# Kernel optimization log

Hardware: AMD Instinct MI355X
Metric: run time of the kernel (lower is better)

The kernel has to match this reference:

```python
import jax, jax.numpy as jnp
import numpy as np

B, C, H, W = 8, 128, 64, 64


def setup_inputs() -> dict:
    key = jax.random.key(0)
    ks = jax.random.split(key, 4)
    s = 1.0 / np.sqrt(C)
    return {
        "x": jax.random.normal(ks[0], (B, C, H, W), dtype=jnp.float32),
        "Wq": jax.random.normal(ks[1], (C, C), dtype=jnp.float32) * s,
        "bq": jnp.zeros((C,), dtype=jnp.float32),
        "Wk": jax.random.normal(ks[2], (C, C), dtype=jnp.float32) * s,
        "bk": jnp.zeros((C,), dtype=jnp.float32),
        "Wv": jax.random.normal(ks[3], (C, C), dtype=jnp.float32) * s,
        "bv": jnp.zeros((C,), dtype=jnp.float32),
    }


def reference(x, Wq, bq, Wk, bk, Wv, bv):
    b, c, h, w = x.shape
    xf = x.reshape(b, c, h * w)  # [B, C, N]
    # 1x1 convs are per-pixel CxC matmuls (weight[out,in] contracted over in)
    q = jnp.einsum("oc,bcn->bon", Wq, xf) + bq[None, :, None]
    k = jnp.einsum("oc,bcn->bon", Wk, xf) + bk[None, :, None]
    v = jnp.einsum("oc,bcn->bon", Wv, xf) + bv[None, :, None]
    scale = 1.0 / jnp.sqrt(jnp.asarray(c, dtype=x.dtype))
    attn = jnp.einsum("bcn,bcm->bnm", q, k) * scale  # [B, N, N]
    attn = jax.nn.softmax(attn, axis=-1)
    out = jnp.einsum("bnm,bcm->bcn", attn, v)  # [B, C, N]
    return out.reshape(b, c, h, w) + x
```

## Files before the change

### kernel.cpp

```cpp
#include <hip/hip_runtime.h>

#define B_ 8
#define C_ 128
#define N_ 4096
#define SCALE 0.08838834764831845f

typedef __attribute__((ext_vector_type(8))) short short8;
typedef __attribute__((ext_vector_type(4))) short short4v;
typedef __attribute__((ext_vector_type(4))) float f32x4;

__device__ inline float b2f(unsigned short u) {
    union { unsigned int i; float f; } v; v.i = ((unsigned int)u) << 16; return v.f;
}
__device__ inline unsigned short f2b(float f) {
    unsigned int x = __float_as_uint(f);
    return (unsigned short)((x + 0x7FFFu + ((x >> 16) & 1u)) >> 16);
}

__device__ inline void gld_lds16(const void* g, void* l) {
    __builtin_amdgcn_global_load_lds(
        (const __attribute__((address_space(1))) unsigned int*)g,
        (__attribute__((address_space(3))) unsigned int*)l, 16, 0, 0);
}

__global__ __launch_bounds__(256) void qkv_mfma(
    const float* __restrict__ x,
    const float* __restrict__ Wq, const float* __restrict__ bq,
    const float* __restrict__ Wk, const float* __restrict__ bk,
    const float* __restrict__ Wv, const float* __restrict__ bv,
    float* __restrict__ q, unsigned short* __restrict__ kTs,
    unsigned short* __restrict__ vS)
{
    __shared__ __align__(16) short Xs[64 * 128];
    __shared__ __align__(16) float Obuf[64 * 132];

    const int t    = threadIdx.x;
    const int w    = t >> 6;
    const int lane = t & 63;
    const int l15  = lane & 15;
    const int quad = lane >> 4;

    const int b  = blockIdx.x & 7;
    const int n0 = (blockIdx.x >> 3) * 64;
    const long base = (long)b * C_ * N_;

    auto load_af = [&](const float* __restrict__ W, short8 (&af)[2][4]) {
        #pragma unroll
        for (int ot = 0; ot < 2; ++ot) {
            const int o = 32 * w + 16 * ot + l15;
            #pragma unroll
            for (int ks = 0; ks < 4; ++ks) {
                const float4 a0 = *(const float4*)(const void*)(W + o * C_ + ks * 32 + quad * 8);
                const float4 a1 = *(const float4*)(const void*)(W + o * C_ + ks * 32 + quad * 8 + 4);
                short8 f;
                f[0] = (short)f2b(a0.x); f[1] = (short)f2b(a0.y);
                f[2] = (short)f2b(a0.z); f[3] = (short)f2b(a0.w);
                f[4] = (short)f2b(a1.x); f[5] = (short)f2b(a1.y);
                f[6] = (short)f2b(a1.z); f[7] = (short)f2b(a1.w);
                af[ot][ks] = f;
            }
        }
    };

    auto mfma_pass = [&](const short8 (&af)[2][4], f32x4 (&acc)[2][4]) {
        #pragma unroll
        for (int ot = 0; ot < 2; ++ot)
            #pragma unroll
            for (int nt = 0; nt < 4; ++nt)
                acc[ot][nt] = (f32x4){0.f, 0.f, 0.f, 0.f};
        #pragma unroll
        for (int nt = 0; nt < 4; ++nt) {
            const int n = nt * 16 + l15;
            short8 bx[4];
            #pragma unroll
            for (int ks = 0; ks < 4; ++ks)
                bx[ks] = *(const short8*)(const void*)(Xs + n * 128 + (((ks * 4 + quad) ^ l15) << 3));
            #pragma unroll
            for (int ot = 0; ot < 2; ++ot)
                #pragma unroll
                for (int ks = 0; ks < 4; ++ks)
                    acc[ot][nt] = __builtin_amdgcn_mfma_f32_16x16x32_bf16(af[ot][ks], bx[ks], acc[ot][nt], 0, 0, 0);
        }
    };

    short8 afA[2][4], afB[2][4];
    load_af(Wq, afA);

    #pragma unroll
    for (int it = 0; it < 8; ++it) {
        const int c  = (t >> 4) + it * 16;
        const int n4 = (t & 15) * 4;
        const float4 xv = *(const float4*)(const void*)(x + base + (long)c * N_ + n0 + n4);
        const int bc = c >> 3, cl = c & 7;
        Xs[(n4 + 0) * 128 + ((bc ^ ((n4 + 0) & 15)) << 3) + cl] = (short)f2b(xv.x);
        Xs[(n4 + 1) * 128 + ((bc ^ ((n4 + 1) & 15)) << 3) + cl] = (short)f2b(xv.y);
        Xs[(n4 + 2) * 128 + ((bc ^ ((n4 + 2) & 15)) << 3) + cl] = (short)f2b(xv.z);
        Xs[(n4 + 3) * 128 + ((bc ^ ((n4 + 3) & 15)) << 3) + cl] = (short)f2b(xv.w);
    }
    __syncthreads();

    {
        load_af(Wv, afB);
        f32x4 acc[2][4];
        mfma_pass(afA, acc);
        #pragma unroll
        for (int ot = 0; ot < 2; ++ot)
            #pragma unroll
            for (int r = 0; r < 4; ++r) {
                const int o = 32 * w + 16 * ot + quad * 4 + r;
                const float bb = bq[o];
                #pragma unroll
                for (int nt = 0; nt < 4; ++nt)
                    q[base + (long)o * N_ + n0 + nt * 16 + l15] = (acc[ot][nt][r] + bb) * SCALE;
            }
    }

    {
        load_af(Wk, afA);
        f32x4 acc[2][4];
        mfma_pass(afB, acc);
        #pragma unroll
        for (int ot = 0; ot < 2; ++ot)
            #pragma unroll
            for (int r = 0; r < 4; ++r) {
                const int o = 32 * w + 16 * ot + quad * 4 + r;
                const float bb = bv[o];
                const int sw = ((o >> 1) & 3) << 3;
                #pragma unroll
                for (int nt = 0; nt < 4; ++nt) {
                    const int n = nt * 16 + l15;
                    const int ns = (n & 32) | ((((n >> 3) & 3) << 3) ^ sw) | (n & 7);
                    vS[base + (long)o * N_ + n0 + ns] = f2b(acc[ot][nt][r] + bb);
                }
            }
    }

    {
        f32x4 acc[2][4];
        mfma_pass(afA, acc);
        #pragma unroll
        for (int ot = 0; ot < 2; ++ot)
            #pragma unroll
            for (int r = 0; r < 4; ++r) {
                const int o = 32 * w + 16 * ot + quad * 4 + r;
                const float bb = bk[o];
                #pragma unroll
                for (int nt = 0; nt < 4; ++nt) {
                    const int n = nt * 16 + l15;
                    Obuf[n * 132 + (((o >> 3) ^ l15) << 3) + (o & 7)] = acc[ot][nt][r] + bb;
                }
            }
        __syncthreads();
        const int n = t >> 2, oh = (t & 3) * 32;
        #pragma unroll
        for (int i = 0; i < 32; i += 4) {
            const float4 kv = *(const float4*)(const void*)(Obuf + n * 132 + oh + i);
            short4v s;
            s[0] = (short)f2b(kv.x); s[1] = (short)f2b(kv.y);
            s[2] = (short)f2b(kv.z); s[3] = (short)f2b(kv.w);
            *(short4v*)(void*)(kTs + base + (long)(n0 + n) * C_ + oh + i) = s;
        }
    }
}

__global__ __launch_bounds__(512) void attn_mfma(
    const float* qg,
    const unsigned short* __restrict__ kTs,
    const unsigned short* __restrict__ vS,
    const float* __restrict__ xg,
    float* out)
{
    __shared__ union {
        struct {
            short K[2][2][4096];
            short V[2][2][4096];
            short Pb[8][16 * 40];
        } s;
        float Ot[64 * 130];
    } sm;
    __shared__ float Ls[2][4][16];
    __shared__ float linvA[64];

    const int t    = threadIdx.x;
    const int w    = t >> 6;
    const int g    = w >> 2;
    const int wq   = w & 3;
    const int lane = t & 63;
    const int l15  = lane & 15;
    const int quad = lane >> 4;

    const int b  = blockIdx.x & 7;
    const int n0 = (blockIdx.x >> 3) * 64;
    const long base = (long)b * C_ * N_;

    const int query = n0 + 16 * wq + l15;
    short8 qf[4];
    #pragma unroll
    for (int ks = 0; ks < 4; ++ks) {
        short8 f;
        #pragma unroll
        for (int j = 0; j < 8; ++j) {
            const int c = ks * 32 + quad * 8 + j;
            f[j] = (short)f2b(qg[base + (long)c * N_ + query]);
        }
        qf[ks] = f;
    }

    f32x4 acc[8];
    #pragma unroll
    for (int ct = 0; ct < 8; ++ct) acc[ct] = (f32x4){0.f, 0.f, 0.f, 0.f};
    f32x4 accS = (f32x4){0.f, 0.f, 0.f, 0.f};
    short8 ones;
    #pragma unroll
    for (int j = 0; j < 8; ++j) ones[j] = (short)0x3F80;

    auto stage = [&](int buf, int pair) {
        const int mt = pair * 2 + g;
        const char* gK = (const char*)(kTs + base + (long)mt * 32 * C_);
        char* lK = (char*)sm.s.K[buf][g];
        char* lV = (char*)sm.s.V[buf][g];
        #pragma unroll
        for (int jj = 0; jj < 2; ++jj) {
            const int d = wq * 2048 + jj * 1024;
            gld_lds16(gK + d + lane * 16, lK + d);
            const int dv = d + lane * 16;
            const int c  = dv >> 6;
            gld_lds16((const char*)(vS + base + (long)c * N_ + mt * 32) + (dv & 63), lV + d);
        }
    };

    auto compute = [&](int buf) {
        const short* Kb = sm.s.K[buf][g];
        const short* Vb = sm.s.V[buf][g];
        f32x4 sc[2];
        sc[0] = (f32x4){0.f, 0.f, 0.f, 0.f};
        sc[1] = (f32x4){0.f, 0.f, 0.f, 0.f};
        #pragma unroll
        for (int kt = 0; kt < 2; ++kt) {
            const int row = (kt * 16 + l15) * 128;
            #pragma unroll
            for (int ks = 0; ks < 4; ++ks) {
                const short8 kf = *(const short8*)(const void*)(Kb + row + (((ks * 4 + quad) ^ l15) << 3));
                sc[kt] = __builtin_amdgcn_mfma_f32_16x16x32_bf16(qf[ks], kf, sc[kt], 0, 0, 0);
            }
        }
        short* Pw = sm.s.Pb[w];
        #pragma unroll
        for (int kt = 0; kt < 2; ++kt)
            #pragma unroll
            for (int r = 0; r < 4; ++r)
                Pw[(quad * 4 + r) * 40 + kt * 16 + l15] = (short)f2b(__expf(sc[kt][r]));
        const short8 pf = *(const short8*)(const void*)(Pw + l15 * 40 + quad * 8);
        accS = __builtin_amdgcn_mfma_f32_16x16x32_bf16(pf, ones, accS, 0, 0, 0);
        #pragma unroll
        for (int ct = 0; ct < 8; ++ct) {
            const short8 vf = *(const short8*)(const void*)(Vb + (ct * 16 + l15) * 32 + ((quad ^ ((l15 >> 1) & 3)) << 3));
            acc[ct] = __builtin_amdgcn_mfma_f32_16x16x32_bf16(pf, vf, acc[ct], 0, 0, 0);
        }
    };

    stage(0, 0);
    __syncthreads();
    for (int i = 0; i < 64; ++i) {
        if (i < 63) stage((i + 1) & 1, i + 1);
        compute(i & 1);
        __syncthreads();
    }

    if (l15 == 0) {
        #pragma unroll
        for (int r = 0; r < 4; ++r) Ls[g][wq][quad * 4 + r] = accS[r];
    }
    if (g == 0) {
        #pragma unroll
        for (int ct = 0; ct < 8; ++ct)
            #pragma unroll
            for (int r = 0; r < 4; ++r)
                sm.Ot[(16 * wq + quad * 4 + r) * 130 + ct * 16 + l15] = acc[ct][r];
    }
    __syncthreads();
    if (g == 1) {
        #pragma unroll
        for (int ct = 0; ct < 8; ++ct)
            #pragma unroll
            for (int r = 0; r < 4; ++r)
                sm.Ot[(16 * wq + quad * 4 + r) * 130 + ct * 16 + l15] += acc[ct][r];
    } else if (l15 == 0) {
        #pragma unroll
        for (int r = 0; r < 4; ++r) {
            const int row = 16 * wq + quad * 4 + r;
            linvA[row] = 1.0f / fmaxf(Ls[0][wq][quad * 4 + r] + Ls[1][wq][quad * 4 + r], 1e-20f);
        }
    }
    __syncthreads();

    const int c  = t >> 2;
    const int nh = (t & 3) * 16;
    const long gb = base + (long)c * N_ + n0 + nh;
    #pragma unroll
    for (int i = 0; i < 16; i += 4) {
        const float4 xs = *(const float4*)(const void*)(xg + gb + i);
        float4 rv;
        rv.x = sm.Ot[(nh + i + 0) * 130 + c] * linvA[nh + i + 0] + xs.x;
        rv.y = sm.Ot[(nh + i + 1) * 130 + c] * linvA[nh + i + 1] + xs.y;
        rv.z = sm.Ot[(nh + i + 2) * 130 + c] * linvA[nh + i + 2] + xs.z;
        rv.w = sm.Ot[(nh + i + 3) * 130 + c] * linvA[nh + i + 3] + xs.w;
        *(float4*)(void*)(out + gb + i) = rv;
    }
}

extern "C" void kernel_launch(void* const* d_in, const int* in_sizes, int n_in,
                              void* d_out, int out_size, void* d_ws, size_t ws_size,
                              hipStream_t stream) {
    const float* x  = (const float*)d_in[0];
    const float* Wq = (const float*)d_in[1];
    const float* bq = (const float*)d_in[2];
    const float* Wk = (const float*)d_in[3];
    const float* bk = (const float*)d_in[4];
    const float* Wv = (const float*)d_in[5];
    const float* bv = (const float*)d_in[6];
    float* out = (float*)d_out;

    const long BCN = (long)B_ * C_ * N_;
    unsigned short* kTs = (unsigned short*)d_ws;
    unsigned short* vS  = kTs + BCN;

    qkv_mfma<<<512, 256, 0, stream>>>(x, Wq, bq, Wk, bk, Wv, bv, out, kTs, vS);
    attn_mfma<<<B_ * (N_ / 64), 512, 0, stream>>>(out, kTs, vS, x, out);
}
```

Baseline: 195.1 us.

## Restructure attention waves to share K/V fragments across two query tiles

Each wave now handles 32 queries and half the key tile (and half the V channels), so one K fragment load feeds two QK MFMAs and one V fragment load feeds two PV MFMAs, reducing LDS traffic per MFMA. Probabilities are exchanged between wave pairs through shared memory with an extra barrier. The scale is premultiplied by log2(e) in the projection kernel so the softmax can use exp2f. The loop also gets manual vmcnt waits, raw s_barrier, setprio hints and a launch-bounds occupancy hint. The extra intra-iteration barrier and the hand-placed waitcnt sequencing add synchronization cost and correctness risk.

```diff
diff --git a/kernel.cpp b/kernel.cpp
--- a/kernel.cpp
+++ b/kernel.cpp
@@ -3,7 +3,7 @@
 #define B_ 8
 #define C_ 128
 #define N_ 4096
-#define SCALE 0.08838834764831845f
+#define SCALE_L2E 0.1275174462578437f
 
 typedef __attribute__((ext_vector_type(8))) short short8;
 typedef __attribute__((ext_vector_type(4))) short short4v;
@@ -111,7 +111,7 @@
                 const float bb = bq[o];
                 #pragma unroll
                 for (int nt = 0; nt < 4; ++nt)
-                    q[base + (long)o * N_ + n0 + nt * 16 + l15] = (acc[ot][nt][r] + bb) * SCALE;
+                    q[base + (long)o * N_ + n0 + nt * 16 + l15] = (acc[ot][nt][r] + bb) * SCALE_L2E;
             }
     }
 
@@ -163,7 +163,7 @@
     }
 }
 
-__global__ __launch_bounds__(512) void attn_mfma(
+__global__ __launch_bounds__(512, 4) void attn_mfma(
     const float* qg,
     const unsigned short* __restrict__ kTs,
     const unsigned short* __restrict__ vS,
@@ -174,17 +174,19 @@
         struct {
             short K[2][2][4096];
             short V[2][2][4096];
-            short Pb[8][16 * 40];
+            short Pb[2][2][32 * 40];
         } s;
         float Ot[64 * 130];
     } sm;
-    __shared__ float Ls[2][4][16];
+    __shared__ float Ls[2][2][32];
     __shared__ float linvA[64];
 
     const int t    = threadIdx.x;
     const int w    = t >> 6;
     const int g    = w >> 2;
-    const int wq   = w & 3;
+    const int wq   = (w >> 1) & 1;
+    const int h    = w & 1;
+    const int sub  = w & 3;
     const int lane = t & 63;
     const int l15  = lane & 15;
     const int quad = lane >> 4;
@@ -193,23 +195,29 @@
     const int n0 = (blockIdx.x >> 3) * 64;
     const long base = (long)b * C_ * N_;
 
-    const int query = n0 + 16 * wq + l15;
-    short8 qf[4];
-    #pragma unroll
-    for (int ks = 0; ks < 4; ++ks) {
-        short8 f;
-        #pragma unroll
-        for (int j = 0; j < 8; ++j) {
-            const int c = ks * 32 + quad * 8 + j;
-            f[j] = (short)f2b(qg[base + (long)c * N_ + query]);
-        }
-        qf[ks] = f;
-    }
-
-    f32x4 acc[8];
-    #pragma unroll
-    for (int ct = 0; ct < 8; ++ct) acc[ct] = (f32x4){0.f, 0.f, 0.f, 0.f};
-    f32x4 accS = (f32x4){0.f, 0.f, 0.f, 0.f};
+    const int query0 = n0 + 32 * wq;
+    short8 qf[2][4];
+    #pragma unroll
+    for (int qh = 0; qh < 2; ++qh)
+        #pragma unroll
+        for (int ks = 0; ks < 4; ++ks) {
+            short8 f;
+            #pragma unroll
+            for (int j = 0; j < 8; ++j) {
+                const int c = ks * 32 + quad * 8 + j;
+                f[j] = (short)f2b(qg[base + (long)c * N_ + query0 + qh * 16 + l15]);
+            }
+            qf[qh][ks] = f;
+        }
+
+    f32x4 acc[2][4];
+    #pragma unroll
+    for (int qh = 0; qh < 2; ++qh)
+        #pragma unroll
+        for (int ct = 0; ct < 4; ++ct) acc[qh][ct] = (f32x4){0.f, 0.f, 0.f, 0.f};
+    f32x4 accS[2];
+    accS[0] = (f32x4){0.f, 0.f, 0.f, 0.f};
+    accS[1] = (f32x4){0.f, 0.f, 0.f, 0.f};
     short8 ones;
     #pragma unroll
     for (int j = 0; j < 8; ++j) ones[j] = (short)0x3F80;
@@ -221,7 +229,7 @@
         char* lV = (char*)sm.s.V[buf][g];
         #pragma unroll
         for (int jj = 0; jj < 2; ++jj) {
-            const int d = wq * 2048 + jj * 1024;
+            const int d = sub * 2048 + jj * 1024;
             gld_lds16(gK + d + lane * 16, lK + d);
             const int dv = d + lane * 16;
             const int c  = dv >> 6;
@@ -229,68 +237,97 @@
         }
     };
 
-    auto compute = [&](int buf) {
+    stage(0, 0);
+    for (int i = 0; i < 64; ++i) {
+        if (i < 63) {
+            stage((i + 1) & 1, i + 1);
+            asm volatile("s_waitcnt vmcnt(4)" ::: "memory");
+        } else {
+            asm volatile("s_waitcnt vmcnt(0)" ::: "memory");
+        }
+        __builtin_amdgcn_s_barrier();
+
+        const int buf = i & 1;
         const short* Kb = sm.s.K[buf][g];
         const short* Vb = sm.s.V[buf][g];
+
+        short8 kf[4];
+        #pragma unroll
+        for (int ks = 0; ks < 4; ++ks)
+            kf[ks] = *(const short8*)(const void*)(Kb + (h * 16 + l15) * 128 + (((ks * 4 + quad) ^ l15) << 3));
         f32x4 sc[2];
         sc[0] = (f32x4){0.f, 0.f, 0.f, 0.f};
         sc[1] = (f32x4){0.f, 0.f, 0.f, 0.f};
-        #pragma unroll
-        for (int kt = 0; kt < 2; ++kt) {
-            const int row = (kt * 16 + l15) * 128;
-            #pragma unroll
-            for (int ks = 0; ks < 4; ++ks) {
-                const short8 kf = *(const short8*)(const void*)(Kb + row + (((ks * 4 + quad) ^ l15) << 3));
-                sc[kt] = __builtin_amdgcn_mfma_f32_16x16x32_bf16(qf[ks], kf, sc[kt], 0, 0, 0);
-            }
-        }
-        short* Pw = sm.s.Pb[w];
-        #pragma unroll
-        for (int kt = 0; kt < 2; ++kt)
+        __builtin_amdgcn_s_setprio(1);
+        #pragma unroll
+        for (int qh = 0; qh < 2; ++qh)
+            #pragma unroll
+            for (int ks = 0; ks < 4; ++ks)
+                sc[qh] = __builtin_amdgcn_mfma_f32_16x16x32_bf16(qf[qh][ks], kf[ks], sc[qh], 0, 0, 0);
+        __builtin_amdgcn_s_setprio(0);
+
+        short* Pw = sm.s.Pb[g][wq];
+        #pragma unroll
+        for (int qh = 0; qh < 2; ++qh)
             #pragma unroll
             for (int r = 0; r < 4; ++r)
-                Pw[(quad * 4 + r) * 40 + kt * 16 + l15] = (short)f2b(__expf(sc[kt][r]));
-        const short8 pf = *(const short8*)(const void*)(Pw + l15 * 40 + quad * 8);
-        accS = __builtin_amdgcn_mfma_f32_16x16x32_bf16(pf, ones, accS, 0, 0, 0);
-        #pragma unroll
-        for (int ct = 0; ct < 8; ++ct) {
-            const short8 vf = *(const short8*)(const void*)(Vb + (ct * 16 + l15) * 32 + ((quad ^ ((l15 >> 1) & 3)) << 3));
-            acc[ct] = __builtin_amdgcn_mfma_f32_16x16x32_bf16(pf, vf, acc[ct], 0, 0, 0);
-        }
-    };
-
-    stage(0, 0);
-    __syncthreads();
-    for (int i = 0; i < 64; ++i) {
-        if (i < 63) stage((i + 1) & 1, i + 1);
-        compute(i & 1);
-        __syncthreads();
-    }
-
-    if (l15 == 0) {
-        #pragma unroll
-        for (int r = 0; r < 4; ++r) Ls[g][wq][quad * 4 + r] = accS[r];
+                Pw[(qh * 16 + quad * 4 + r) * 40 + h * 16 + l15] = (short)f2b(exp2f(sc[qh][r]));
+
+        asm volatile("s_waitcnt lgkmcnt(0)" ::: "memory");
+        __builtin_amdgcn_s_barrier();
+        __builtin_amdgcn_sched_barrier(0);
+
+        const short8 pf0 = *(const short8*)(const void*)(Pw + (l15) * 40 + quad * 8);
+        const short8 pf1 = *(const short8*)(const void*)(Pw + (16 + l15) * 40 + quad * 8);
+        __builtin_amdgcn_s_setprio(1);
+        if (h == 0) {
+            accS[0] = __builtin_amdgcn_mfma_f32_16x16x32_bf16(pf0, ones, accS[0], 0, 0, 0);
+            accS[1] = __builtin_amdgcn_mfma_f32_16x16x32_bf16(pf1, ones, accS[1], 0, 0, 0);
+        }
+        #pragma unroll
+        for (int ct = 0; ct < 4; ++ct) {
+            const int ch = h * 64 + ct * 16 + l15;
+            const short8 vf = *(const short8*)(const void*)(Vb + ch * 32 + ((quad ^ ((l15 >> 1) & 3)) << 3));
+            acc[0][ct] = __builtin_amdgcn_mfma_f32_16x16x32_bf16(pf0, vf, acc[0][ct], 0, 0, 0);
+            acc[1][ct] = __builtin_amdgcn_mfma_f32_16x16x32_bf16(pf1, vf, acc[1][ct], 0, 0, 0);
+        }
+        __builtin_amdgcn_s_setprio(0);
+        __builtin_amdgcn_s_barrier();
+    }
+
+    if (h == 0 && l15 == 0) {
+        #pragma unroll
+        for (int qh = 0; qh < 2; ++qh)
+            #pragma unroll
+            for (int r = 0; r < 4; ++r)
+                Ls[g][wq][qh * 16 + quad * 4 + r] = accS[qh][r];
     }
     if (g == 0) {
         #pragma unroll
-        for (int ct = 0; ct < 8; ++ct)
-            #pragma unroll
-            for (int r = 0; r < 4; ++r)
-                sm.Ot[(16 * wq + quad * 4 + r) * 130 + ct * 16 + l15] = acc[ct][r];
+        for (int qh = 0; qh < 2; ++qh)
+            #pragma unroll
+            for (int ct = 0; ct < 4; ++ct)
+                #pragma unroll
+                for (int r = 0; r < 4; ++r)
+                    sm.Ot[(32 * wq + qh * 16 + quad * 4 + r) * 130 + h * 64 + ct * 16 + l15] = acc[qh][ct][r];
     }
     __syncthreads();
     if (g == 1) {
         #pragma unroll
-        for (int ct = 0; ct < 8; ++ct)
-            #pragma unroll
-            for (int r = 0; r < 4; ++r)
-                sm.Ot[(16 * wq + quad * 4 + r) * 130 + ct * 16 + l15] += acc[ct][r];
-    } else if (l15 == 0) {
-        #pragma unroll
-        for (int r = 0; r < 4; ++r) {
-            const int row = 16 * wq + quad * 4 + r;
-            linvA[row] = 1.0f / fmaxf(Ls[0][wq][quad * 4 + r] + Ls[1][wq][quad * 4 + r], 1e-20f);
-        }
+        for (int qh = 0; qh < 2; ++qh)
+            #pragma unroll
+            for (int ct = 0; ct < 4; ++ct)
+                #pragma unroll
+                for (int r = 0; r < 4; ++r)
+                    sm.Ot[(32 * wq + qh * 16 + quad * 4 + r) * 130 + h * 64 + ct * 16 + l15] += acc[qh][ct][r];
+    } else if (h == 0 && l15 == 0) {
+        #pragma unroll
+        for (int qh = 0; qh < 2; ++qh)
+            #pragma unroll
+            for (int r = 0; r < 4; ++r) {
+                const int r32 = qh * 16 + quad * 4 + r;
+                linvA[32 * wq + r32] = 1.0f / fmaxf(Ls[0][wq][r32] + Ls[1][wq][r32], 1e-20f);
+            }
     }
     __syncthreads();
 
```

Measured after the change: 198.2 us. About the same (+1.6%).
